# Kernel optimization log

Measured on AMD Instinct MI355X. Metric: run time of the kernel, lower is better.

The kernel has to match this reference:

```python
import jax, jax.numpy as jnp
import numpy as np

K = 3
KK = K * K


def _conv1x1(x, w, b):
    # x: [B,Ci,H,W], w: [Co,Ci]
    return jnp.einsum('bihw,oi->bohw', x, w) + b[None, :, None, None]


def _conv3x3(x, w, b):
    y = jax.lax.conv_general_dilated(x, w, (1, 1), ((1, 1), (1, 1)),
                                     dimension_numbers=('NCHW', 'OIHW', 'NCHW'))
    return y + b[None, :, None, None]


def _deform_conv3x3(x, offset, w, b):
    # Deformable conv v1, kernel 3x3, stride 1, pad 1, dilation 1, 1 deformable group.
    # x: [B,C,H,W]; offset: [B,2*KK,H,W] (dy,dx interleaved per kernel tap); w: [Co,C,3,3]
    B, C, H, W = x.shape
    dt = x.dtype
    off = offset.reshape(B, KK, 2, H, W)
    ky, kx = jnp.meshgrid(jnp.arange(K, dtype=dt), jnp.arange(K, dtype=dt), indexing='ij')
    ky = ky.reshape(KK)
    kx = kx.reshape(KK)
    # sampling locations: out_pos - pad + kernel_tap + learned offset
    base_y = jnp.arange(H, dtype=dt) - 1.0  # pad = 1
    base_x = jnp.arange(W, dtype=dt) - 1.0
    sy = base_y[None, None, :, None] + ky[None, :, None, None] + off[:, :, 0]  # [B,KK,H,W]
    sx = base_x[None, None, None, :] + kx[None, :, None, None] + off[:, :, 1]
    y0 = jnp.floor(sy)
    x0 = jnp.floor(sx)
    ty = sy - y0
    tx = sx - x0

    def gather(iy, ix):
        valid = ((iy >= 0) & (iy <= H - 1) & (ix >= 0) & (ix <= W - 1)).astype(dt)
        iyc = jnp.clip(iy, 0, H - 1).astype(jnp.int32)
        ixc = jnp.clip(ix, 0, W - 1).astype(jnp.int32)
        vals = jax.vmap(lambda img, a, c: img[:, a, c])(x, iyc, ixc)  # [B,C,KK,H,W]
        return vals * valid[:, None]

    w00 = ((1 - ty) * (1 - tx))[:, None]
    w01 = ((1 - ty) * tx)[:, None]
    w10 = (ty * (1 - tx))[:, None]
    w11 = (ty * tx)[:, None]
    sampled = (gather(y0, x0) * w00 + gather(y0, x0 + 1) * w01 +
               gather(y0 + 1, x0) * w10 + gather(y0 + 1, x0 + 1) * w11)  # [B,C,KK,H,W]
    Co = w.shape[0]
    out = jnp.einsum('bikhw,oik->bohw', sampled, w.reshape(Co, C, KK))
    return out + b[None, :, None, None]


def _branch(features, dw, db, ow, ob, tw, tb):
    h = _conv1x1(features, dw, db)
    off = _conv3x3(h, ow, ob)  # offset-predicting conv inside DFConv2d
    return jax.nn.relu(_deform_conv3x3(h, off, tw, tb))


def setup_inputs() -> dict:
    key = jax.random.key(0)
    ks = jax.random.split(key, 13)
    C = 256
    s1 = 1.0 / np.sqrt(C)          # kaiming_normal a=1 for 1x1 conv
    s3 = 1.0 / np.sqrt(C * KK)     # 3x3 conv
    so = 0.01                       # small offset-conv weights -> modest offsets
    f = lambda k, s, sc: jax.random.normal(k, s, dtype=jnp.float32) * sc
    return {
        'features': f(ks[0], (4, C, 64, 64), 1.0),
        'agg_down_w': f(ks[1], (C, C), s1),
        'agg_down_b': jnp.zeros((C,), jnp.float32),
        'agg_off_w': f(ks[2], (2 * KK, C, K, K), so),
        'agg_off_b': jnp.zeros((2 * KK,), jnp.float32),
        'agg_w': f(ks[3], (C, C, K, K), s3),
        'agg_b': jnp.zeros((C,), jnp.float32),
        'appr_down_w': f(ks[4], (C, C), s1),
        'appr_down_b': jnp.zeros((C,), jnp.float32),
        'appr_off_w': f(ks[5], (2 * KK, C, K, K), so),
        'appr_off_b': jnp.zeros((2 * KK,), jnp.float32),
        'appr_w': f(ks[6], (C, C, K, K), s3),
        'appr_b': jnp.zeros((C,), jnp.float32),
    }


def reference(features, agg_down_w, agg_down_b, agg_off_w, agg_off_b, agg_w, agg_b,
              appr_down_w, appr_down_b, appr_off_w, appr_off_b, appr_w, appr_b):
    agg = _branch(features, agg_down_w, agg_down_b, agg_off_w, agg_off_b, agg_w, agg_b)
    appr = _branch(features, appr_down_w, appr_down_b, appr_off_w, appr_off_b, appr_w, appr_b)
    return (agg, appr)
```

## Files before the change

kernel.cpp:

```cpp
#include <hip/hip_runtime.h>

#define HWP 4096
#define NPIX 4194304
#define KDIM 2304

typedef __attribute__((ext_vector_type(4))) float f32x4;
typedef __attribute__((ext_vector_type(4))) int   i32x4;
typedef __attribute__((ext_vector_type(8))) short short8;
typedef __attribute__((ext_vector_type(4))) unsigned short bf16x4;
typedef __attribute__((ext_vector_type(4))) unsigned short u16x4;

__device__ __forceinline__ unsigned short bf16_rne(float f) {
    unsigned int u = __builtin_bit_cast(unsigned int, f);
    u += 0x7FFFu + ((u >> 16) & 1u);
    return (unsigned short)(u >> 16);
}

__device__ __forceinline__ float bf2f(unsigned short u) {
    return __builtin_bit_cast(float, (unsigned int)u << 16);
}

__device__ __forceinline__ float u2f_lo(unsigned int u) {
    return __builtin_bit_cast(float, u << 16);
}

__device__ __forceinline__ float u2f_hi(unsigned int u) {
    return __builtin_bit_cast(float, u & 0xFFFF0000u);
}

__device__ __forceinline__ unsigned int cvt_pk_bf16(float lo, float hi) {
    unsigned int r;
    asm("v_cvt_pk_bf16_f32 %0, %1, %2" : "=v"(r) : "v"(lo), "v"(hi));
    return r;
}

__device__ __forceinline__ void gload_lds16(const void* g, void* l) {
    __builtin_amdgcn_global_load_lds((const __attribute__((address_space(1))) void*)g,
                                     (__attribute__((address_space(3))) void*)l, 16, 0, 0);
}

__device__ __forceinline__ f32x4 ntld_f4(const float* p) {
    return __builtin_nontemporal_load(reinterpret_cast<const f32x4*>(p));
}
__device__ __forceinline__ u16x4 ntld_u4(const unsigned short* p) {
    return __builtin_nontemporal_load(reinterpret_cast<const u16x4*>(p));
}

__global__ void prep_all_kernel(const float* __restrict__ x, unsigned short* __restrict__ fbt,
                                const float* __restrict__ dw0, const float* __restrict__ dw1,
                                const float* __restrict__ tw0, const float* __restrict__ tw1,
                                const float* __restrict__ ow0, const float* __restrict__ ow1,
                                unsigned short* __restrict__ w1b2,
                                unsigned short* __restrict__ w2A,
                                unsigned short* __restrict__ w2o) {
    __shared__ float T[64][65];
    int b = blockIdx.x;
    int t = threadIdx.x;
    if (b < 1024) {
        int pt = b & 63, ct = (b >> 6) & 3, bb = b >> 8;
        int lane = t & 63;
        int w = t >> 6;
        int c0 = ct * 64, p0 = pt * 64;
        const float* xb = x + (size_t)(bb * 256 + c0) * HWP + p0;
#pragma unroll
        for (int j = 0; j < 4; ++j) {
            int ci = w * 16 + j * 4 + (lane >> 4);
            int px = (lane & 15) * 4;
            float4 v = *reinterpret_cast<const float4*>(xb + (size_t)ci * HWP + px);
            T[ci][px]     = v.x;
            T[ci][px + 1] = v.y;
            T[ci][px + 2] = v.z;
            T[ci][px + 3] = v.w;
        }
        __syncthreads();
        unsigned short* ob = fbt + ((size_t)bb * HWP + p0) * 256 + c0;
#pragma unroll
        for (int j = 0; j < 4; ++j) {
            int px  = w * 16 + j * 4 + (lane >> 4);
            int ci4 = (lane & 15) * 4;
            bf16x4 o4;
            o4[0] = bf16_rne(T[ci4 + 0][px]);
            o4[1] = bf16_rne(T[ci4 + 1][px]);
            o4[2] = bf16_rne(T[ci4 + 2][px]);
            o4[3] = bf16_rne(T[ci4 + 3][px]);
            *reinterpret_cast<bf16x4*>(ob + (size_t)px * 256 + ci4) = o4;
        }
        return;
    }
    int idx = (b - 1024) * 256 + t;
    if (idx < 131072) {
        int br = idx >> 16;
        int i  = idx & 65535;
        const float* dw = br ? dw1 : dw0;
        w1b2[idx] = bf16_rne(dw[i]);
    } else if (idx < 131072 + 1179648) {
        int j = idx - 131072;
        int br = j >= 589824;
        int i  = br ? j - 589824 : j;
        const float* tw = br ? tw1 : tw0;
        int cg = i / 147456;
        int r  = i - cg * 147456;
        int tap = r >> 14;
        int r2 = r & 16383;
        int s  = r2 >> 11;
        int fr = (r2 >> 9) & 3;
        int l  = (r2 >> 3) & 63;
        int e  = r2 & 7;
        int o  = cg * 64 + fr * 16 + (l & 15);
        int ci = s * 32 + ((l >> 4) << 3) + e;
        w2A[j] = bf16_rne(tw[(o * 256 + ci) * 9 + tap]);
    } else {
        int j = idx - 131072 - 1179648;
        int br = j >= 73728;
        int i  = br ? j - 73728 : j;
        const float* ow = br ? ow1 : ow0;
        int m = i / 2304;
        int k = i - m * 2304;
        int tap = k >> 8;
        int ci  = k & 255;
        w2o[j] = (m < 18) ? bf16_rne(ow[(m * 256 + ci) * 9 + tap]) : (unsigned short)0;
    }
}

__global__ void prep_w2_kernel(const float* __restrict__ tw0, const float* __restrict__ tw1,
                               unsigned short* __restrict__ w2) {
    int idx = blockIdx.x * 256 + threadIdx.x;
    int br = idx >= 589824;
    int i  = br ? idx - 589824 : idx;
    const float* tw = br ? tw1 : tw0;
    int ci = i & 255;
    int r  = i >> 8;
    int tap = r % 9;
    int o   = r / 9;
    w2[idx] = bf16_rne(tw[(o * 256 + ci) * 9 + tap]);
}

__global__ void prep_ow2_kernel(const float* __restrict__ ow0, const float* __restrict__ ow1,
                                float* __restrict__ owt) {
    int idx = blockIdx.x * 256 + threadIdx.x;
    int br = idx >= 41472;
    int i  = br ? idx - 41472 : idx;
    const float* ow = br ? ow1 : ow0;
    int co = i % 18;
    int r  = i / 18;
    int k  = r % 9;
    int ci = r / 9;
    owt[idx] = ow[(co * 256 + ci) * 9 + k];
}

__global__ void prep_w12_kernel(const float* __restrict__ dw0, const float* __restrict__ dw1,
                                unsigned short* __restrict__ w1b) {
    int idx = blockIdx.x * 256 + threadIdx.x;
    int br = idx >> 16;
    int i  = idx & 65535;
    const float* dw = br ? dw1 : dw0;
    w1b[idx] = bf16_rne(dw[i]);
}

__global__ void prep_fb16_kernel(const float* __restrict__ x, unsigned short* __restrict__ fbt) {
    __shared__ float T[64][65];
    int pt = blockIdx.x;
    int ct = blockIdx.y;
    int bb = blockIdx.z;
    int t = threadIdx.x;
    int lane = t & 63;
    int r = t >> 6;
    int c0 = ct * 64, p0 = pt * 64;
    const float* xb = x + (size_t)(bb * 256 + c0) * HWP + p0;
#pragma unroll
    for (int rr = 0; rr < 16; ++rr) {
        int ci = r * 16 + rr;
        T[ci][lane] = xb[(size_t)ci * HWP + lane];
    }
    __syncthreads();
    unsigned short* ob = fbt + ((size_t)bb * HWP + p0) * 256 + c0;
#pragma unroll
    for (int rr = 0; rr < 16; ++rr) {
        int px = r * 16 + rr;
        ob[(size_t)px * 256 + lane] = bf16_rne(T[lane][px]);
    }
}

__launch_bounds__(256)
__global__ void gemm1x1_kernel(const unsigned short* __restrict__ w1b2,
                               const unsigned short* __restrict__ fbt,
                               const float* __restrict__ db0, const float* __restrict__ db1,
                               float* __restrict__ h2, unsigned short* __restrict__ ht2,
                               int write_h) {
    __shared__ unsigned short As[128 * 64];
    __shared__ unsigned short Bs[64 * 64];
    int pt = blockIdx.x;
    int ot = blockIdx.y;
    int z  = blockIdx.z;
    int bb = z & 3;
    int br = z >> 2;
    const unsigned short* w1b = w1b2 + (size_t)br * 65536;
    const float* db = br ? db1 : db0;
    int t  = threadIdx.x;
    int l  = t & 63;
    int w  = t >> 6;
    int wr = w >> 1, wc = w & 1;
    int o0 = ot * 128, p0 = pt * 64;
    const unsigned short* fb = fbt + (size_t)bb * HWP * 256;
    f32x4 acc[4][2];
#pragma unroll
    for (int i = 0; i < 4; ++i)
#pragma unroll
        for (int j = 0; j < 2; ++j) acc[i][j] = (f32x4){0.f, 0.f, 0.f, 0.f};

    for (int ks = 0; ks < 4; ++ks) {
        int k0 = ks * 64;
#pragma unroll
        for (int rA = 0; rA < 4; ++rA) {
            int s = rA * 256 + t;
            int row = s >> 3, cg = (s & 7) ^ (row & 7);
            gload_lds16(w1b + (size_t)(o0 + row) * 256 + k0 + cg * 8, As + s * 8);
        }
#pragma unroll
        for (int rB = 0; rB < 2; ++rB) {
            int s = rB * 256 + t;
            int row = s >> 3, cg = (s & 7) ^ (row & 7);
            gload_lds16(fb + (size_t)(p0 + row) * 256 + k0 + cg * 8, Bs + s * 8);
        }
        __syncthreads();
#pragma unroll
        for (int half = 0; half < 2; ++half) {
            short8 a[4], b[2];
#pragma unroll
            for (int fr = 0; fr < 4; ++fr) {
                int row = wr * 64 + fr * 16 + (l & 15);
                int oct = half * 4 + (l >> 4);
                a[fr] = *reinterpret_cast<const short8*>(As + row * 64 + ((oct ^ (row & 7)) * 8));
            }
#pragma unroll
            for (int fc = 0; fc < 2; ++fc) {
                int row = wc * 32 + fc * 16 + (l & 15);
                int oct = half * 4 + (l >> 4);
                b[fc] = *reinterpret_cast<const short8*>(Bs + row * 64 + ((oct ^ (row & 7)) * 8));
            }
#pragma unroll
            for (int fr = 0; fr < 4; ++fr)
#pragma unroll
                for (int fc = 0; fc < 2; ++fc)
                    acc[fr][fc] = __builtin_amdgcn_mfma_f32_16x16x32_bf16(a[fr], b[fc], acc[fr][fc], 0, 0, 0);
        }
        __syncthreads();
    }

    float* hb = h2 + (size_t)br * NPIX + (size_t)bb * 256 * HWP;
    unsigned short* htb = ht2 + (size_t)br * NPIX + (size_t)bb * HWP * 256;
#pragma unroll
    for (int fr = 0; fr < 4; ++fr) {
        int o = o0 + wr * 64 + fr * 16 + ((l >> 4) << 2);
#pragma unroll
        for (int fc = 0; fc < 2; ++fc) {
            int p = p0 + wc * 32 + fc * 16 + (l & 15);
            f32x4 v;
#pragma unroll
            for (int reg = 0; reg < 4; ++reg) {
                v[reg] = acc[fr][fc][reg] + db[o + reg];
                if (write_h) hb[(size_t)(o + reg) * HWP + p] = v[reg];
            }
            uint2 pk;
            pk.x = cvt_pk_bf16(v[0], v[1]);
            pk.y = cvt_pk_bf16(v[2], v[3]);
            *reinterpret_cast<uint2*>(htb + (size_t)p * 256 + o) = pk;
        }
    }
}

__launch_bounds__(256)
__global__ void off_mfma_kernel(const unsigned short* __restrict__ w2o,
                                const unsigned short* __restrict__ ht2,
                                const float* __restrict__ ob0, const float* __restrict__ ob1,
                                float* __restrict__ dwq, unsigned short* __restrict__ dcq) {
    __shared__ float red[4][1152];
    int id = blockIdx.x;
    int br = id >> 8;
    int bb = (id >> 6) & 3;
    int y  = id & 63;
    const unsigned short* wA = w2o + (size_t)br * 73728;
    const unsigned short* htb = ht2 + (size_t)br * NPIX + (size_t)bb * HWP * 256;
    const float* ob = br ? ob1 : ob0;
    int t = threadIdx.x;
    int l = t & 63;
    int w = t >> 6;
    short8 zero = {};
    f32x4 acc[2][4];
#pragma unroll
    for (int i = 0; i < 2; ++i)
#pragma unroll
        for (int j = 0; j < 4; ++j) acc[i][j] = (f32x4){0.f, 0.f, 0.f, 0.f};

    for (int tap = 0; tap < 9; ++tap) {
        int ky = tap / 3, kx = tap % 3;
        int yy = y + ky - 1;
        bool vy = (yy >= 0) && (yy < 64);
        int cyy = min(max(yy, 0), 63);
#pragma unroll
        for (int sh = 0; sh < 2; ++sh) {
            int s = w * 2 + sh;
            short8 a[2], b[4];
#pragma unroll
            for (int fr = 0; fr < 2; ++fr)
                a[fr] = *reinterpret_cast<const short8*>(
                    wA + (size_t)(fr * 16 + (l & 15)) * KDIM + tap * 256 + s * 32 + ((l >> 4) << 3));
#pragma unroll
            for (int fc = 0; fc < 4; ++fc) {
                int px = fc * 16 + (l & 15);
                int xx = px + kx - 1;
                bool v = vy && (xx >= 0) && (xx < 64);
                int cxx = min(max(xx, 0), 63);
                short8 bv = *reinterpret_cast<const short8*>(
                    htb + (size_t)(cyy * 64 + cxx) * 256 + s * 32 + ((l >> 4) << 3));
                b[fc] = v ? bv : zero;
            }
#pragma unroll
            for (int fr = 0; fr < 2; ++fr)
#pragma unroll
                for (int fc = 0; fc < 4; ++fc)
                    acc[fr][fc] = __builtin_amdgcn_mfma_f32_16x16x32_bf16(a[fr], b[fc], acc[fr][fc], 0, 0, 0);
        }
    }

#pragma unroll
    for (int fr = 0; fr < 2; ++fr)
#pragma unroll
        for (int fc = 0; fc < 4; ++fc) {
            int px = fc * 16 + (l & 15);
#pragma unroll
            for (int reg = 0; reg < 4; ++reg) {
                int co = fr * 16 + ((l >> 4) << 2) + reg;
                if (co < 18) red[w][co * 64 + px] = acc[fr][fc][reg];
            }
        }
    __syncthreads();

    size_t dbase = ((size_t)(br * 4 + bb) * 9) * 4096 + (size_t)(y * 64);
    for (int e = t; e < 576; e += 256) {
        int tap = e >> 6, px = e & 63;
        int c0 = 2 * tap, c1 = 2 * tap + 1;
        float dy = ob[c0] + red[0][c0 * 64 + px] + red[1][c0 * 64 + px]
                          + red[2][c0 * 64 + px] + red[3][c0 * 64 + px];
        float dx = ob[c1] + red[0][c1 * 64 + px] + red[1][c1 * 64 + px]
                          + red[2][c1 * 64 + px] + red[3][c1 * 64 + px];
        int ky = tap / 3, kx = tap % 3;
        float sy = (float)(y - 1 + ky) + dy;
        float sx = (float)(px - 1 + kx) + dx;
        float y0f = floorf(sy), x0f = floorf(sx);
        float ty = sy - y0f, tx = sx - x0f;
        int iy0 = (int)y0f, ix0 = (int)x0f;
        int iy1 = iy0 + 1, ix1 = ix0 + 1;
        bool vy0 = (iy0 >= 0) & (iy0 < 64);
        bool vy1 = (iy1 >= 0) & (iy1 < 64);
        bool vx0 = (ix0 >= 0) & (ix0 < 64);
        bool vx1 = (ix1 >= 0) & (ix1 < 64);
        int cy0 = min(max(iy0, 0), 63), cy1 = min(max(iy1, 0), 63);
        int cx0 = min(max(ix0, 0), 63), cx1 = min(max(ix1, 0), 63);
        f32x4 ww;
        ww[0] = (1.f - ty) * (1.f - tx) * ((vy0 & vx0) ? 1.f : 0.f);
        ww[1] = (1.f - ty) * tx * ((vy0 & vx1) ? 1.f : 0.f);
        ww[2] = ty * (1.f - tx) * ((vy1 & vx0) ? 1.f : 0.f);
        ww[3] = ty * tx * ((vy1 & vx1) ? 1.f : 0.f);
        u16x4 pc;
        pc[0] = (unsigned short)(cy0 * 64 + cx0);
        pc[1] = (unsigned short)(cy0 * 64 + cx1);
        pc[2] = (unsigned short)(cy1 * 64 + cx0);
        pc[3] = (unsigned short)(cy1 * 64 + cx1);
        size_t di = dbase + (size_t)tap * 4096 + px;
        *reinterpret_cast<f32x4*>(dwq + di * 4) = ww;
        *reinterpret_cast<u16x4*>(dcq + di * 4) = pc;
    }
}

__global__ void off_conv_part_kernel(const float* __restrict__ h2, const float* __restrict__ owt2,
                                     float* __restrict__ part2) {
    int y  = blockIdx.x & 63;
    int bb = blockIdx.x >> 6;
    int c  = blockIdx.y;
    int br = blockIdx.z;
    const float* h = h2 + (size_t)br * NPIX;
    const float* owt = owt2 + (size_t)br * 41472;
    float* part = part2 + (size_t)br * 2359296;
    int t  = threadIdx.x;
    int x  = t & 63;
    int wv = __builtin_amdgcn_readfirstlane(t >> 6);
    int  toff[9];
    bool tval[9];
#pragma unroll
    for (int ky = 0; ky < 3; ++ky) {
        int yy = y + ky - 1;
        bool vy = (yy >= 0) && (yy < 64);
        int cyy = min(max(yy, 0), 63);
#pragma unroll
        for (int kx = 0; kx < 3; ++kx) {
            int xx = x + kx - 1;
            tval[ky * 3 + kx] = vy && (xx >= 0) && (xx < 64);
            toff[ky * 3 + kx] = cyy * 64 + min(max(xx, 0), 63);
        }
    }
    float acc[18];
#pragma unroll
    for (int co = 0; co < 18; ++co) acc[co] = 0.f;
    int ci0 = c * 32 + wv * 8;
    const float* hb = h + (size_t)(bb * 256 + ci0) * HWP;
#pragma unroll
    for (int i = 0; i < 8; ++i) {
        const float* hc = hb + i * HWP;
        const float* wci = owt + (size_t)(ci0 + i) * 162;
#pragma unroll
        for (int k = 0; k < 9; ++k) {
            float hv = hc[toff[k]];
            hv = tval[k] ? hv : 0.f;
            const float* wk = wci + k * 18;
#pragma unroll
            for (int co = 0; co < 18; ++co)
                acc[co] = fmaf(wk[co], hv, acc[co]);
        }
    }
    __shared__ float red[4][18][64];
    int wvl = t >> 6;
#pragma unroll
    for (int co = 0; co < 18; ++co) red[wvl][co][x] = acc[co];
    __syncthreads();
    if (wvl == 0) {
#pragma unroll
        for (int co = 0; co < 18; ++co) {
            float s = red[0][co][x] + red[1][co][x] + red[2][co][x] + red[3][co][x];
            part[(size_t)c * 294912 + ((bb * 18 + co) << 12) + (y << 6) + x] = s;
        }
    }
}

__global__ void off_reduce2_kernel(const float* __restrict__ part2,
                                   const float* __restrict__ ob0, const float* __restrict__ ob1,
                                   float* __restrict__ off2) {
    int idx = blockIdx.x * 256 + threadIdx.x;
    int br = idx >= 294912;
    int i  = br ? idx - 294912 : idx;
    const float* part = part2 + (size_t)br * 2359296;
    const float* b = br ? ob1 : ob0;
    int co = (i >> 12) % 18;
    float s = b[co];
#pragma unroll
    for (int c = 0; c < 8; ++c) s += part[(size_t)c * 294912 + i];
    off2[idx] = s;
}

__launch_bounds__(256, 2)
__global__ void dgemm_fused_kernel(const unsigned short* __restrict__ w2b,
                                   const unsigned short* __restrict__ ht2,
                                   const float* __restrict__ dwq,
                                   const unsigned short* __restrict__ dcq,
                                   const float* __restrict__ tb0,
                                   const float* __restrict__ tb1,
                                   float* __restrict__ out) {
    __shared__ unsigned short Bs[2][64 * 256];
    int id = blockIdx.x;
    int sw = (id & 7) * 64 + (id >> 3);
    int br = sw >> 8;
    int mt = sw & 255;
    int bb = mt >> 6;
    int y  = mt & 63;
    const unsigned short* w2f = w2b + (size_t)br * 589824;
    const unsigned short* htb = ht2 + (size_t)br * NPIX + (size_t)bb * HWP * 256;
    const float* bias = br ? tb1 : tb0;
    size_t dbase = ((size_t)(br * 4 + bb) * 9) * 4096 + (size_t)(y * 64);
    int t = threadIdx.x;
    int l = t & 63;
    int w = t >> 6;
    int wvu = __builtin_amdgcn_readfirstlane(w);
    int le = l << 2;

    f32x4 acc[4][4];
#pragma unroll
    for (int i = 0; i < 4; ++i)
#pragma unroll
        for (int j = 0; j < 4; ++j) acc[i][j] = (f32x4){0.f, 0.f, 0.f, 0.f};

#define STAGE_B(TAPV, WB)                                                          \
    do {                                                                           \
        const float* dwt = dwq + (dbase + (size_t)(TAPV) * 4096) * 4;              \
        const unsigned short* dct = dcq + (dbase + (size_t)(TAPV) * 4096) * 4;     \
        _Pragma("unroll")                                                          \
        for (int i_ = 0; i_ < 16; ++i_) {                                          \
            int px = wvu * 16 + i_;                                                \
            f32x4 ww = ntld_f4(dwt + (size_t)px * 4);                              \
            u16x4 pc = ntld_u4(dct + (size_t)px * 4);                              \
            int b00 = ((int)pc[0] << 8) + le;                                      \
            int b01 = ((int)pc[1] << 8) + le;                                      \
            int b10 = ((int)pc[2] << 8) + le;                                      \
            int b11 = ((int)pc[3] << 8) + le;                                      \
            uint2 u00 = *reinterpret_cast<const uint2*>(htb + b00);                \
            uint2 u01 = *reinterpret_cast<const uint2*>(htb + b01);                \
            uint2 u10 = *reinterpret_cast<const uint2*>(htb + b10);                \
            uint2 u11 = *reinterpret_cast<const uint2*>(htb + b11);                \
            float s0 = fmaf(ww[0], u2f_lo(u00.x),                                  \
                       fmaf(ww[1], u2f_lo(u01.x),                                  \
                       fmaf(ww[2], u2f_lo(u10.x), ww[3] * u2f_lo(u11.x))));        \
            float s1 = fmaf(ww[0], u2f_hi(u00.x),                                  \
                       fmaf(ww[1], u2f_hi(u01.x),                                  \
                       fmaf(ww[2], u2f_hi(u10.x), ww[3] * u2f_hi(u11.x))));        \
            float s2 = fmaf(ww[0], u2f_lo(u00.y),                                  \
                       fmaf(ww[1], u2f_lo(u01.y),                                  \
                       fmaf(ww[2], u2f_lo(u10.y), ww[3] * u2f_lo(u11.y))));        \
            float s3 = fmaf(ww[0], u2f_hi(u00.y),                                  \
                       fmaf(ww[1], u2f_hi(u01.y),                                  \
                       fmaf(ww[2], u2f_hi(u10.y), ww[3] * u2f_hi(u11.y))));        \
            uint2 pk;                                                              \
            pk.x = cvt_pk_bf16(s0, s1);                                            \
            pk.y = cvt_pk_bf16(s2, s3);                                            \
            int g = l >> 1, sub = l & 1;                                           \
            *reinterpret_cast<uint2*>((WB) + px * 256 +                            \
                (((g ^ (px & 7)) << 3) | (sub << 2))) = pk;                        \
        }                                                                          \
    } while (0)

#define COMPUTE_TAP(TAPV, RB)                                                      \
    do {                                                                           \
        const unsigned short* wtapf = w2f + (size_t)(wvu * 9 + (TAPV)) * 16384;    \
        short8 aA[4], aB[4];                                                       \
        _Pragma("unroll")                                                          \
        for (int fr = 0; fr < 4; ++fr)                                             \
            aA[fr] = *reinterpret_cast<const short8*>(wtapf + fr * 512 + (l << 3));\
        _Pragma("unroll")                                                          \
        for (int fr = 0; fr < 4; ++fr)                                             \
            aB[fr] = *reinterpret_cast<const short8*>(wtapf + (4 + fr) * 512 + (l << 3)); \
        _Pragma("unroll")                                                          \
        for (int s = 0; s < 8; ++s) {                                              \
            short8 aC[4];                                                          \
            if (s < 6) {                                                           \
                _Pragma("unroll")                                                  \
                for (int fr = 0; fr < 4; ++fr)                                     \
                    aC[fr] = *reinterpret_cast<const short8*>(                     \
                        wtapf + (size_t)((s + 2) * 4 + fr) * 512 + (l << 3));      \
            }                                                                      \
            short8 b[4];                                                           \
            _Pragma("unroll")                                                      \
            for (int fc = 0; fc < 4; ++fc) {                                       \
                int prow = fc * 16 + (l & 15);                                     \
                int cg8 = (s << 2) + (l >> 4);                                     \
                b[fc] = *reinterpret_cast<const short8*>(                          \
                    (RB) + prow * 256 + ((cg8 ^ (prow & 7)) << 3));                \
            }                                                                      \
            __builtin_amdgcn_s_setprio(1);                                         \
            _Pragma("unroll")                                                      \
            for (int fr = 0; fr < 4; ++fr)                                         \
                _Pragma("unroll")                                                  \
                for (int fc = 0; fc < 4; ++fc)                                     \
                    acc[fr][fc] = __builtin_amdgcn_mfma_f32_16x16x32_bf16(         \
                        aA[fr], b[fc], acc[fr][fc], 0, 0, 0);                      \
            __builtin_amdgcn_s_setprio(0);                                         \
            if (s < 7) {                                                           \
                _Pragma("unroll")                                                  \
                for (int fr = 0; fr < 4; ++fr) { aA[fr] = aB[fr]; aB[fr] = aC[fr]; } \
            }                                                                      \
        }                                                                          \
    } while (0)

    STAGE_B(0, Bs[0]);
    __syncthreads();
#pragma unroll 1
    for (int it = 0; it < 4; ++it) {
        int tap = it * 2;
        COMPUTE_TAP(tap, Bs[0]);
        STAGE_B(tap + 1, Bs[1]);
        __syncthreads();
        COMPUTE_TAP(tap + 1, Bs[1]);
        STAGE_B(tap + 2, Bs[0]);
        __syncthreads();
    }
    COMPUTE_TAP(8, Bs[0]);
#undef STAGE_B
#undef COMPUTE_TAP

    float* outp = out + (size_t)br * NPIX + (size_t)(bb * 256) * HWP + y * 64;
#pragma unroll
    for (int fr = 0; fr < 4; ++fr) {
        int o = wvu * 64 + fr * 16 + ((l >> 4) << 2);
#pragma unroll
        for (int fc = 0; fc < 4; ++fc) {
            int pxc = fc * 16 + (l & 15);
#pragma unroll
            for (int reg = 0; reg < 4; ++reg) {
                float v = acc[fr][fc][reg] + bias[o + reg];
                outp[(size_t)(o + reg) * HWP + pxc] = fmaxf(v, 0.f);
            }
        }
    }
}

__launch_bounds__(256)
__global__ void sample2_kernel(const unsigned short* __restrict__ ht, const float* __restrict__ off,
                               unsigned short* __restrict__ sm, int b0) {
    int y   = blockIdx.x;
    int tap = blockIdx.y;
    int bb  = b0 + blockIdx.z;
    int t   = threadIdx.x;
    int lane = t & 63;
    int wv  = t >> 6;
    int ky = tap / 3, kx = tap % 3;
    const unsigned short* htb = ht + (size_t)bb * HWP * 256;
    const float* offy = off + ((bb * 18 + 2 * tap) * 64 + y) * 64;
    const float* offx = off + ((bb * 18 + 2 * tap + 1) * 64 + y) * 64;
    int mrow = ((bb - b0) * 64 + y) * 64;
#pragma unroll 4
    for (int i = 0; i < 16; ++i) {
        int px = wv * 16 + i;
        float dy = offy[px];
        float dx = offx[px];
        float sy = (float)(y - 1 + ky) + dy;
        float sx = (float)(px - 1 + kx) + dx;
        float y0f = floorf(sy), x0f = floorf(sx);
        float ty = sy - y0f, tx = sx - x0f;
        int iy0 = (int)y0f, ix0 = (int)x0f;
        int iy1 = iy0 + 1, ix1 = ix0 + 1;
        bool vy0 = (iy0 >= 0) & (iy0 < 64);
        bool vy1 = (iy1 >= 0) & (iy1 < 64);
        bool vx0 = (ix0 >= 0) & (ix0 < 64);
        bool vx1 = (ix1 >= 0) & (ix1 < 64);
        int cy0 = min(max(iy0, 0), 63), cy1 = min(max(iy1, 0), 63);
        int cx0 = min(max(ix0, 0), 63), cx1 = min(max(ix1, 0), 63);
        float w00 = (1.f - ty) * (1.f - tx) * ((vy0 & vx0) ? 1.f : 0.f);
        float w01 = (1.f - ty) * tx * ((vy0 & vx1) ? 1.f : 0.f);
        float w10 = ty * (1.f - tx) * ((vy1 & vx0) ? 1.f : 0.f);
        float w11 = ty * tx * ((vy1 & vx1) ? 1.f : 0.f);
        int le = lane << 2;
        bf16x4 q00 = *reinterpret_cast<const bf16x4*>(htb + ((cy0 * 64 + cx0) << 8) + le);
        bf16x4 q01 = *reinterpret_cast<const bf16x4*>(htb + ((cy0 * 64 + cx1) << 8) + le);
        bf16x4 q10 = *reinterpret_cast<const bf16x4*>(htb + ((cy1 * 64 + cx0) << 8) + le);
        bf16x4 q11 = *reinterpret_cast<const bf16x4*>(htb + ((cy1 * 64 + cx1) << 8) + le);
        f32x4 s;
#pragma unroll
        for (int j = 0; j < 4; ++j)
            s[j] = fmaf(w00, bf2f(q00[j]),
                   fmaf(w01, bf2f(q01[j]),
                   fmaf(w10, bf2f(q10[j]), w11 * bf2f(q11[j]))));
        uint2 pk;
        pk.x = cvt_pk_bf16(s[0], s[1]);
        pk.y = cvt_pk_bf16(s[2], s[3]);
        *reinterpret_cast<uint2*>(sm + (size_t)(mrow + px) * KDIM + tap * 256 + lane * 4) = pk;
    }
}

__launch_bounds__(256)
__global__ void gemm2_kernel(const unsigned short* __restrict__ w2b,
                             const unsigned short* __restrict__ smb, size_t smstride,
                             const float* __restrict__ tb0, const float* __restrict__ tb1,
                             float* __restrict__ out, int mbase) {
    __shared__ unsigned short As[128 * 64];
    __shared__ unsigned short Bs[64 * 64];
    int mt = blockIdx.x;
    int ot = blockIdx.y;
    int br = blockIdx.z;
    const unsigned short* w2 = w2b + (size_t)br * 589824;
    const unsigned short* sm = smb + (size_t)br * smstride;
    const float* bias = br ? tb1 : tb0;
    float* outp = out + (size_t)br * NPIX;
    int t  = threadIdx.x;
    int l  = t & 63;
    int w  = t >> 6;
    int wr = w >> 1, wc = w & 1;
    int o0 = ot * 128, m0 = mt * 64;
    f32x4 acc[4][2];
#pragma unroll
    for (int i = 0; i < 4; ++i)
#pragma unroll
        for (int j = 0; j < 2; ++j) acc[i][j] = (f32x4){0.f, 0.f, 0.f, 0.f};

    for (int ks = 0; ks < KDIM / 64; ++ks) {
        int k0 = ks * 64;
#pragma unroll
        for (int rA = 0; rA < 4; ++rA) {
            int s = rA * 256 + t;
            int row = s >> 3, cg = (s & 7) ^ (row & 7);
            gload_lds16(w2 + (size_t)(o0 + row) * KDIM + k0 + cg * 8, As + s * 8);
        }
#pragma unroll
        for (int rB = 0; rB < 2; ++rB) {
            int s = rB * 256 + t;
            int row = s >> 3, cg = (s & 7) ^ (row & 7);
            gload_lds16(sm + (size_t)(m0 + row) * KDIM + k0 + cg * 8, Bs + s * 8);
        }
        __syncthreads();
#pragma unroll
        for (int half = 0; half < 2; ++half) {
            short8 a[4], b[2];
#pragma unroll
            for (int fr = 0; fr < 4; ++fr) {
                int row = wr * 64 + fr * 16 + (l & 15);
                int oct = half * 4 + (l >> 4);
                a[fr] = *reinterpret_cast<const short8*>(As + row * 64 + ((oct ^ (row & 7)) * 8));
            }
#pragma unroll
            for (int fc = 0; fc < 2; ++fc) {
                int row = wc * 32 + fc * 16 + (l & 15);
                int oct = half * 4 + (l >> 4);
                b[fc] = *reinterpret_cast<const short8*>(Bs + row * 64 + ((oct ^ (row & 7)) * 8));
            }
#pragma unroll
            for (int fr = 0; fr < 4; ++fr)
#pragma unroll
                for (int fc = 0; fc < 2; ++fc)
                    acc[fr][fc] = __builtin_amdgcn_mfma_f32_16x16x32_bf16(a[fr], b[fc], acc[fr][fc], 0, 0, 0);
        }
        __syncthreads();
    }

#pragma unroll
    for (int fr = 0; fr < 4; ++fr) {
        int o = o0 + wr * 64 + fr * 16 + ((l >> 4) << 2);
#pragma unroll
        for (int fc = 0; fc < 2; ++fc) {
            int mg = mbase + m0 + wc * 32 + fc * 16 + (l & 15);
            int bbv = mg >> 12;
            int pix = mg & 4095;
            float* op = outp + (size_t)(bbv * 256) * HWP + pix;
#pragma unroll
            for (int reg = 0; reg < 4; ++reg) {
                float v = acc[fr][fc][reg] + bias[o + reg];
                op[(size_t)(o + reg) * HWP] = fmaxf(v, 0.f);
            }
        }
    }
}

extern "C" void kernel_launch(void* const* d_in, const int* in_sizes, int n_in,
                              void* d_out, int out_size, void* d_ws, size_t ws_size,
                              hipStream_t stream) {
    const float* feat = (const float*)d_in[0];
    char* base = (char*)d_ws;
    float* outp = (float*)d_out;
    const size_t perb = (size_t)HWP * KDIM * 2;

    const float* dw0 = (const float*)d_in[1];
    const float* db0 = (const float*)d_in[2];
    const float* ow0 = (const float*)d_in[3];
    const float* ob0 = (const float*)d_in[4];
    const float* tw0 = (const float*)d_in[5];
    const float* tb0 = (const float*)d_in[6];
    const float* dw1 = (const float*)d_in[7];
    const float* db1 = (const float*)d_in[8];
    const float* ow1 = (const float*)d_in[9];
    const float* ob1 = (const float*)d_in[10];
    const float* tw1 = (const float*)d_in[11];
    const float* tb1 = (const float*)d_in[12];

    bool tierA = ws_size >= 47218688;

    if (tierA) {
        unsigned short* ht2 = (unsigned short*)base;
        unsigned short* w2A = (unsigned short*)(base + 35913728);
        unsigned short* w2o = (unsigned short*)(base + 38273024);
        unsigned short* fbt = (unsigned short*)(base + 38567936);
        unsigned short* w1b2 = (unsigned short*)(base + 46956544);
        float* dwq = (float*)(base + 38567936);
        unsigned short* dcq = (unsigned short*)(base + 38567936 + 4718592);

        hipLaunchKernelGGL(prep_all_kernel, dim3(6720), dim3(256), 0, stream,
                           feat, fbt, dw0, dw1, tw0, tw1, ow0, ow1, w1b2, w2A, w2o);
        hipLaunchKernelGGL(gemm1x1_kernel, dim3(64, 2, 8), dim3(256), 0, stream,
                           w1b2, fbt, db0, db1, (float*)nullptr, ht2, 0);
        hipLaunchKernelGGL(off_mfma_kernel, dim3(512), dim3(256), 0, stream,
                           w2o, ht2, ob0, ob1, dwq, dcq);
        hipLaunchKernelGGL(dgemm_fused_kernel, dim3(512), dim3(256), 0, stream,
                           w2A, ht2, dwq, dcq, tb0, tb1, outp);
        return;
    }

    float* h   = (float*)base;
    float* off = h + NPIX;
    unsigned short* w2 = (unsigned short*)(base + 17956864);
    float* owt = (float*)(base + 19136512);
    unsigned short* ht = (unsigned short*)(base + 19302400);
    unsigned short* smN = (unsigned short*)(base + 27691008);
    float* partN = (float*)(base + 27691008);
    unsigned short* fbtN = (unsigned short*)(base + 27691008 + 9437184);
    unsigned short* w1bN = (unsigned short*)(base + 27691008 + 17825792);

    int nb = 0;
    if (27691008 + 4 * perb <= ws_size) nb = 4;
    else if (27691008 + 2 * perb <= ws_size) nb = 2;
    else nb = 1;

    for (int br = 0; br < 2; ++br) {
        const float* dw = (const float*)d_in[1 + 6 * br];
        const float* db = (const float*)d_in[2 + 6 * br];
        const float* ow = (const float*)d_in[3 + 6 * br];
        const float* ob = (const float*)d_in[4 + 6 * br];
        const float* tw = (const float*)d_in[5 + 6 * br];
        const float* tb = (const float*)d_in[6 + 6 * br];

        hipLaunchKernelGGL(prep_fb16_kernel, dim3(64, 4, 4), dim3(256), 0, stream, feat, fbtN);
        hipLaunchKernelGGL(prep_w12_kernel, dim3(256), dim3(256), 0, stream, dw, dw, w1bN);
        hipLaunchKernelGGL(gemm1x1_kernel, dim3(64, 2, 4), dim3(256), 0, stream,
                           w1bN, fbtN, db, db, h, ht, 1);
        hipLaunchKernelGGL(prep_ow2_kernel, dim3(162), dim3(256), 0, stream, ow, ow, owt);
        hipLaunchKernelGGL(off_conv_part_kernel, dim3(256, 8, 1), dim3(256), 0, stream,
                           h, owt, partN);
        hipLaunchKernelGGL(off_reduce2_kernel, dim3(1152), dim3(256), 0, stream,
                           partN, ob, ob, off);
        hipLaunchKernelGGL(prep_w2_kernel, dim3(2304), dim3(256), 0, stream, tw, tw, w2);

        for (int b0 = 0; b0 < 4; b0 += nb) {
            hipLaunchKernelGGL(sample2_kernel, dim3(64, 9, nb), dim3(256), 0, stream,
                               ht, off, smN, b0);
            hipLaunchKernelGGL(gemm2_kernel, dim3(nb * 64, 2, 1), dim3(256), 0, stream,
                               w2, smN, (size_t)0, tb, tb, outp + br * NPIX, b0 * HWP);
        }
    }
}
```

Baseline: 121.6 us.

## Fuse feature fp32-to-bf16 transpose into the 1x1 conv GEMM

Removes the separate transpose/convert pass that wrote a bf16 channel-last copy of the features, and has a new 1x1 GEMM kernel read fp32 features directly, converting to bf16 while filling LDS. Each block now covers all 256 output channels for 64 pixels, so features are read once per branch instead of per output tile. This avoids the extra global write and read of the transposed buffer, but uses strided scalar fp32 loads and a larger LDS tile, which may lower occupancy.

```diff
diff --git a/kernel.cpp b/kernel.cpp
--- a/kernel.cpp
+++ b/kernel.cpp
@@ -46,48 +46,13 @@
     return __builtin_nontemporal_load(reinterpret_cast<const u16x4*>(p));
 }
 
-__global__ void prep_all_kernel(const float* __restrict__ x, unsigned short* __restrict__ fbt,
-                                const float* __restrict__ dw0, const float* __restrict__ dw1,
+__global__ void prep_all_kernel(const float* __restrict__ dw0, const float* __restrict__ dw1,
                                 const float* __restrict__ tw0, const float* __restrict__ tw1,
                                 const float* __restrict__ ow0, const float* __restrict__ ow1,
                                 unsigned short* __restrict__ w1b2,
                                 unsigned short* __restrict__ w2A,
                                 unsigned short* __restrict__ w2o) {
-    __shared__ float T[64][65];
-    int b = blockIdx.x;
-    int t = threadIdx.x;
-    if (b < 1024) {
-        int pt = b & 63, ct = (b >> 6) & 3, bb = b >> 8;
-        int lane = t & 63;
-        int w = t >> 6;
-        int c0 = ct * 64, p0 = pt * 64;
-        const float* xb = x + (size_t)(bb * 256 + c0) * HWP + p0;
-#pragma unroll
-        for (int j = 0; j < 4; ++j) {
-            int ci = w * 16 + j * 4 + (lane >> 4);
-            int px = (lane & 15) * 4;
-            float4 v = *reinterpret_cast<const float4*>(xb + (size_t)ci * HWP + px);
-            T[ci][px]     = v.x;
-            T[ci][px + 1] = v.y;
-            T[ci][px + 2] = v.z;
-            T[ci][px + 3] = v.w;
-        }
-        __syncthreads();
-        unsigned short* ob = fbt + ((size_t)bb * HWP + p0) * 256 + c0;
-#pragma unroll
-        for (int j = 0; j < 4; ++j) {
-            int px  = w * 16 + j * 4 + (lane >> 4);
-            int ci4 = (lane & 15) * 4;
-            bf16x4 o4;
-            o4[0] = bf16_rne(T[ci4 + 0][px]);
-            o4[1] = bf16_rne(T[ci4 + 1][px]);
-            o4[2] = bf16_rne(T[ci4 + 2][px]);
-            o4[3] = bf16_rne(T[ci4 + 3][px]);
-            *reinterpret_cast<bf16x4*>(ob + (size_t)px * 256 + ci4) = o4;
-        }
-        return;
-    }
-    int idx = (b - 1024) * 256 + t;
+    int idx = blockIdx.x * 256 + threadIdx.x;
     if (idx < 131072) {
         int br = idx >> 16;
         int i  = idx & 65535;
@@ -178,6 +143,95 @@
     for (int rr = 0; rr < 16; ++rr) {
         int px = r * 16 + rr;
         ob[(size_t)px * 256 + lane] = bf16_rne(T[lane][px]);
+    }
+}
+
+__launch_bounds__(256)
+__global__ void gemm1x1f_kernel(const unsigned short* __restrict__ w1b2,
+                                const float* __restrict__ feat,
+                                const float* __restrict__ db0, const float* __restrict__ db1,
+                                unsigned short* __restrict__ ht2) {
+    __shared__ unsigned short As[256 * 64];
+    __shared__ unsigned short Bs[64 * 64];
+    int pt = blockIdx.x;
+    int z  = blockIdx.y;
+    int bb = z & 3;
+    int br = z >> 2;
+    const unsigned short* w1b = w1b2 + (size_t)br * 65536;
+    const float* db = br ? db1 : db0;
+    int t = threadIdx.x;
+    int l = t & 63;
+    int w = t >> 6;
+    int p0 = pt * 64;
+    const float* xb = feat + (size_t)(bb * 256) * HWP;
+    f32x4 acc[4][4];
+#pragma unroll
+    for (int i = 0; i < 4; ++i)
+#pragma unroll
+        for (int j = 0; j < 4; ++j) acc[i][j] = (f32x4){0.f, 0.f, 0.f, 0.f};
+
+    for (int ks = 0; ks < 4; ++ks) {
+        int k0 = ks * 64;
+#pragma unroll
+        for (int rA = 0; rA < 8; ++rA) {
+            int s = rA * 256 + t;
+            int row = s >> 3, cg = (s & 7) ^ (row & 7);
+            gload_lds16(w1b + (size_t)row * 256 + k0 + cg * 8, As + s * 8);
+        }
+        {
+            const float* src = xb + (size_t)(k0 + w * 16) * HWP + p0 + l;
+            float f[16];
+#pragma unroll
+            for (int i = 0; i < 16; ++i) f[i] = src[(size_t)i * HWP];
+            uint4 q0, q1;
+            q0.x = cvt_pk_bf16(f[0], f[1]);   q0.y = cvt_pk_bf16(f[2], f[3]);
+            q0.z = cvt_pk_bf16(f[4], f[5]);   q0.w = cvt_pk_bf16(f[6], f[7]);
+            q1.x = cvt_pk_bf16(f[8], f[9]);   q1.y = cvt_pk_bf16(f[10], f[11]);
+            q1.z = cvt_pk_bf16(f[12], f[13]); q1.w = cvt_pk_bf16(f[14], f[15]);
+            *reinterpret_cast<uint4*>(Bs + l * 64 + (((w * 2) ^ (l & 7)) << 3)) = q0;
+            *reinterpret_cast<uint4*>(Bs + l * 64 + (((w * 2 + 1) ^ (l & 7)) << 3)) = q1;
+        }
+        __syncthreads();
+#pragma unroll
+        for (int half = 0; half < 2; ++half) {
+            short8 a[4], b[4];
+#pragma unroll
+            for (int fr = 0; fr < 4; ++fr) {
+                int row = w * 64 + fr * 16 + (l & 15);
+                int oct = half * 4 + (l >> 4);
+                a[fr] = *reinterpret_cast<const short8*>(As + row * 64 + ((oct ^ (row & 7)) * 8));
+            }
+#pragma unroll
+            for (int fc = 0; fc < 4; ++fc) {
+                int row = fc * 16 + (l & 15);
+                int oct = half * 4 + (l >> 4);
+                b[fc] = *reinterpret_cast<const short8*>(Bs + row * 64 + ((oct ^ (row & 7)) * 8));
+            }
+#pragma unroll
+            for (int fr = 0; fr < 4; ++fr)
+#pragma unroll
+                for (int fc = 0; fc < 4; ++fc)
+                    acc[fr][fc] = __builtin_amdgcn_mfma_f32_16x16x32_bf16(a[fr], b[fc], acc[fr][fc], 0, 0, 0);
+        }
+        __syncthreads();
+    }
+
+    unsigned short* htb = ht2 + (size_t)br * NPIX + (size_t)bb * HWP * 256;
+#pragma unroll
+    for (int fr = 0; fr < 4; ++fr) {
+        int o = w * 64 + fr * 16 + ((l >> 4) << 2);
+#pragma unroll
+        for (int fc = 0; fc < 4; ++fc) {
+            int p = p0 + fc * 16 + (l & 15);
+            f32x4 v;
+#pragma unroll
+            for (int reg = 0; reg < 4; ++reg)
+                v[reg] = acc[fr][fc][reg] + db[o + reg];
+            uint2 pk;
+            pk.x = cvt_pk_bf16(v[0], v[1]);
+            pk.y = cvt_pk_bf16(v[2], v[3]);
+            *reinterpret_cast<uint2*>(htb + (size_t)p * 256 + o) = pk;
+        }
     }
 }
 
@@ -752,15 +806,14 @@
         unsigned short* ht2 = (unsigned short*)base;
         unsigned short* w2A = (unsigned short*)(base + 35913728);
         unsigned short* w2o = (unsigned short*)(base + 38273024);
-        unsigned short* fbt = (unsigned short*)(base + 38567936);
         unsigned short* w1b2 = (unsigned short*)(base + 46956544);
         float* dwq = (float*)(base + 38567936);
         unsigned short* dcq = (unsigned short*)(base + 38567936 + 4718592);
 
-        hipLaunchKernelGGL(prep_all_kernel, dim3(6720), dim3(256), 0, stream,
-                           feat, fbt, dw0, dw1, tw0, tw1, ow0, ow1, w1b2, w2A, w2o);
-        hipLaunchKernelGGL(gemm1x1_kernel, dim3(64, 2, 8), dim3(256), 0, stream,
-                           w1b2, fbt, db0, db1, (float*)nullptr, ht2, 0);
+        hipLaunchKernelGGL(prep_all_kernel, dim3(5696), dim3(256), 0, stream,
+                           dw0, dw1, tw0, tw1, ow0, ow1, w1b2, w2A, w2o);
+        hipLaunchKernelGGL(gemm1x1f_kernel, dim3(64, 8), dim3(256), 0, stream,
+                           w1b2, feat, db0, db1, ht2);
         hipLaunchKernelGGL(off_mfma_kernel, dim3(512), dim3(256), 0, stream,
                            w2o, ht2, ob0, ob1, dwq, dcq);
         hipLaunchKernelGGL(dgemm_fused_kernel, dim3(512), dim3(256), 0, stream,
```

Measured after the change: 124.8 us. 1.03x slower.
